# Kernel tuning notes

Hardware: AMD Instinct MI355X
Metric: run time of the kernel (lower is better)

The kernel has to match this reference:

```python
import jax, jax.numpy as jnp
import numpy as np

N_NODES = 50000
N_EDGES = 800000
D = 128          # input_dim == output_dim
H = 2 * D        # hidden size = 2*output_dim
EPS = 1e-5       # BatchNorm1d eps


def _mlp(x, W1, b1, g1, beta1, W2, b2):
    # Linear -> BatchNorm1d (training-mode batch stats) -> ReLU -> Linear
    y = x @ W1 + b1
    mu = jnp.mean(y, axis=0)
    var = jnp.mean(jnp.square(y - mu), axis=0)  # biased var, as used for normalization
    y = (y - mu) * jax.lax.rsqrt(var + EPS) * g1 + beta1
    y = jax.nn.relu(y)
    return y @ W2 + b2


def setup_inputs() -> dict:
    key = jax.random.key(0)
    ks = jax.random.split(key, 16)
    h = jax.random.normal(ks[0], (N_NODES, D), dtype=jnp.float32)
    e = jax.random.normal(ks[1], (N_EDGES, D), dtype=jnp.float32)
    src = jax.random.randint(ks[2], (N_EDGES,), 0, N_NODES, dtype=jnp.int32)
    dst = jax.random.randint(ks[3], (N_EDGES,), 0, N_NODES, dtype=jnp.int32)

    def lin(k, fan_in, fan_out):
        return jax.random.normal(k, (fan_in, fan_out), dtype=jnp.float32) * (1.0 / np.sqrt(fan_in))

    params = {
        # mlp_bond: in 2D -> H -> D
        'W1b': lin(ks[4], 2 * D, H), 'b1b': jnp.zeros((H,), jnp.float32),
        'g1b': jnp.ones((H,), jnp.float32), 'beta1b': jnp.zeros((H,), jnp.float32),
        'W2b': lin(ks[5], H, D), 'b2b': jnp.zeros((D,), jnp.float32),
        # mlp_atom: in 2D -> H -> D
        'W1a': lin(ks[6], 2 * D, H), 'b1a': jnp.zeros((H,), jnp.float32),
        'g1a': jnp.ones((H,), jnp.float32), 'beta1a': jnp.zeros((H,), jnp.float32),
        'W2a': lin(ks[7], H, D), 'b2a': jnp.zeros((D,), jnp.float32),
    }
    return {'h': h, 'e': e, 'src': src, 'dst': dst, **params}


def reference(h, e, src, dst,
              W1b, b1b, g1b, beta1b, W2b, b2b,
              W1a, b1a, g1a, beta1a, W2a, b2a):
    # --- bond update: gather u_add_v, concat with e, MLP ---
    sum_h_edge = h[src] + h[dst]                              # [E, D]
    e_new = _mlp(jnp.concatenate([sum_h_edge, e], axis=-1),
                 W1b, b1b, g1b, beta1b, W2b, b2b)             # [E, D]

    # --- atom update: scatter-sum of src node feats and NEW edge feats to dst ---
    sum_h = jax.ops.segment_sum(h[src], dst, num_segments=N_NODES)   # copy_u + sum
    sum_e = jax.ops.segment_sum(e_new, dst, num_segments=N_NODES)   # copy_e + sum
    h_new = _mlp(jnp.concatenate([sum_h, sum_e], axis=-1),
                 W1a, b1a, g1a, beta1a, W2a, b2a)             # [N, D]

    # out_batch_norm=False, out_activation=None, residual=False, dropout=None
    return h_new, e_new
```

## Files before the change

### kernel.cpp

```cpp
#include <hip/hip_runtime.h>
#include <stdint.h>

#define DD 128
#define HH 256
#define EPSBN 1e-5f

typedef __attribute__((ext_vector_type(4))) float f32x4;
typedef __attribute__((ext_vector_type(8))) short s16x8;
typedef __attribute__((ext_vector_type(4))) short s16x4;

__device__ __forceinline__ unsigned short f2bf(float f){
  union{float f; unsigned u;} v; v.f=f;
  unsigned u = v.u + 0x7fffu + ((v.u>>16)&1u);
  return (unsigned short)(u>>16);
}
__device__ __forceinline__ float bf2f(unsigned short s){
  union{unsigned u; float f;} v; v.u=((unsigned)s)<<16; return v.f;
}
__device__ __forceinline__ int swz(int row, int kb){ return row*512 + (kb ^ ((row&7)<<4)); }

__global__ void wt_kernel(const float* __restrict__ W1b, const float* __restrict__ W2b,
                          const float* __restrict__ W1a, const float* __restrict__ W2a,
                          unsigned short* __restrict__ WT1b, unsigned short* __restrict__ WT2b,
                          unsigned short* __restrict__ WT1a, unsigned short* __restrict__ WT2a){
  int idx = blockIdx.x*256 + threadIdx.x;
  if (idx < 65536){ int n=idx>>8, k=idx&255; WT1b[n*256+k]=f2bf(W1b[k*256+n]); }
  else if (idx < 98304){ int t=idx-65536; int n=t>>8, k=t&255; WT2b[n*256+k]=f2bf(W2b[k*128+n]); }
  else if (idx < 163840){ int t=idx-98304; int n=t>>8, k=t&255; WT1a[n*256+k]=f2bf(W1a[k*256+n]); }
  else if (idx < 196608){ int t=idx-163840; int n=t>>8, k=t&255; WT2a[n*256+k]=f2bf(W2a[k*128+n]); }
}

__global__ void h2bf_kernel(const float* __restrict__ h, unsigned short* __restrict__ hb, int n8){
  int i = blockIdx.x*256 + threadIdx.x;
  if (i < n8){
    f32x4 a = *(const f32x4*)(h + (size_t)i*8);
    f32x4 b = *(const f32x4*)(h + (size_t)i*8 + 4);
    s16x8 p;
    #pragma unroll
    for (int q=0;q<4;q++){ p[q]=(short)f2bf(a[q]); p[4+q]=(short)f2bf(b[q]); }
    *(s16x8*)(hb + (size_t)i*8) = p;
  }
}

__global__ void hist_kernel(const int* __restrict__ dst, int* __restrict__ counts, int E){
  int i = blockIdx.x*256 + threadIdx.x;
  if (i < E) atomicAdd(&counts[dst[i]], 1);
}

__global__ void scan_kernel(const int* __restrict__ counts, int* __restrict__ offsets,
                            int* __restrict__ cursor, int n){
  __shared__ int wsum[16];
  int tid = threadIdx.x, lane = tid&63, wid = tid>>6;
  int carry = 0;
  int nch = (n + 1023)/1024;
  for (int ch=0; ch<nch; ch++){
    int i = ch*1024 + tid;
    int v = (i<n)? counts[i] : 0;
    int s = v;
    #pragma unroll
    for (int off=1; off<64; off<<=1){ int t = __shfl_up(s, off); if (lane>=off) s += t; }
    if (lane==63) wsum[wid] = s;
    __syncthreads();
    int woff = 0, tot = 0;
    #pragma unroll
    for (int w=0; w<16; w++){ int t = wsum[w]; if (w<wid) woff += t; tot += t; }
    if (i<n){ int excl = carry + woff + s - v; offsets[i]=excl; cursor[i]=excl; }
    carry += tot;
    __syncthreads();
  }
  if (tid==0) offsets[n] = carry;
}

__global__ void fill_kernel(const int* __restrict__ dst, int* __restrict__ cursor,
                            int* __restrict__ eids, int E){
  int i = blockIdx.x*256 + threadIdx.x;
  if (i < E){ int slot = atomicAdd(&cursor[dst[i]], 1); eids[slot] = i; }
}

__global__ __launch_bounds__(512, 4) void edge_mlp1_stream(
    const unsigned short* __restrict__ hb, const float* __restrict__ e,
    const int* __restrict__ src, const int* __restrict__ dstv,
    const unsigned short* __restrict__ WT1, const float* __restrict__ b1,
    unsigned short* __restrict__ yout, float* __restrict__ stats,
    int E, int ntiles)
{
  __shared__ alignas(16) char xt[32768];
  const int tid = threadIdx.x;
  const int l = tid&63, w = tid>>6, lr = l&15, lg = l>>4;
  const int nb = w*32;

  s16x8 Bf[8][2];
  #pragma unroll
  for (int kc=0;kc<8;kc++)
    #pragma unroll
    for (int nt=0;nt<2;nt++)
      Bf[kc][nt] = *(const s16x8*)(WT1 + (size_t)(nb + nt*16 + lr)*256 + kc*32 + lg*8);
  float bias0 = b1[nb+lr], bias1 = b1[nb+16+lr];

  float st1a=0.f, st1b=0.f, st2a=0.f, st2b=0.f;

  for (int t = blockIdx.x; t < ntiles; t += gridDim.x){
    const int base = t*64;
    {
      const int cb = tid&31, r0 = tid>>5;
      #pragma unroll
      for (int k=0;k<4;k++){
        int r = r0 + k*16;
        f32x4 v = *(const f32x4*)(e + (size_t)(base+r)*DD + cb*4);
        s16x4 p;
        #pragma unroll
        for (int q=0;q<4;q++) p[q] = (short)f2bf(v[q]);
        *(s16x4*)(xt + swz(r, 256 + cb*8)) = p;
      }
    }
    {
      const int r = tid>>3, jj = tid&7;
      const int ei = base + r;
      int s_ = src[ei], d_ = dstv[ei];
      const s16x8* hs = (const s16x8*)(hb + (size_t)s_*DD) + jj*2;
      const s16x8* hd = (const s16x8*)(hb + (size_t)d_*DD) + jj*2;
      s16x8 a0=hs[0], a1=hs[1], c0=hd[0], c1=hd[1];
      s16x8 o0, o1;
      #pragma unroll
      for (int q=0;q<8;q++){
        o0[q] = (short)f2bf(bf2f((unsigned short)a0[q]) + bf2f((unsigned short)c0[q]));
        o1[q] = (short)f2bf(bf2f((unsigned short)a1[q]) + bf2f((unsigned short)c1[q]));
      }
      *(s16x8*)(xt + swz(r, jj*32))      = o0;
      *(s16x8*)(xt + swz(r, jj*32 + 16)) = o1;
    }
    __syncthreads();
    f32x4 acc[4][2];
    #pragma unroll
    for (int mt=0;mt<4;mt++)
      #pragma unroll
      for (int nt=0;nt<2;nt++) acc[mt][nt] = (f32x4){0.f,0.f,0.f,0.f};
    #pragma unroll
    for (int kc=0;kc<8;kc++){
      s16x8 af[4];
      #pragma unroll
      for (int mt=0;mt<4;mt++)
        af[mt] = *(const s16x8*)(xt + swz(mt*16 + lr, kc*64 + lg*16));
      #pragma unroll
      for (int nt=0;nt<2;nt++)
        #pragma unroll
        for (int mt=0;mt<4;mt++)
          acc[mt][nt] = __builtin_amdgcn_mfma_f32_16x16x32_bf16(af[mt], Bf[kc][nt], acc[mt][nt], 0,0,0);
    }
    #pragma unroll
    for (int mt=0;mt<4;mt++)
      #pragma unroll
      for (int q=0;q<4;q++){
        float v0 = acc[mt][0][q] + bias0;
        float v1 = acc[mt][1][q] + bias1;
        st1a += v0; st2a += v0*v0;
        st1b += v1; st2b += v1*v1;
      }
    __syncthreads();
    #pragma unroll
    for (int mt=0;mt<4;mt++)
      #pragma unroll
      for (int q=0;q<4;q++){
        *(unsigned short*)(xt + (mt*16 + lg*4 + q)*512 + (nb + lr)*2)      = f2bf(acc[mt][0][q] + bias0);
        *(unsigned short*)(xt + (mt*16 + lg*4 + q)*512 + (nb + 16 + lr)*2) = f2bf(acc[mt][1][q] + bias1);
      }
    __syncthreads();
    #pragma unroll
    for (int it=0;it<4;it++){
      int off = it*8192 + tid*16;
      *(s16x8*)((char*)yout + (size_t)base*512 + off) = *(const s16x8*)(xt + off);
    }
    __syncthreads();
  }
  {
    int rep = blockIdx.x & 63;
    float s;
    s = st1a; s += __shfl_xor(s,16); s += __shfl_xor(s,32);
    if (l < 16) atomicAdd(&stats[rep*512 + nb + lr], s);
    s = st2a; s += __shfl_xor(s,16); s += __shfl_xor(s,32);
    if (l < 16) atomicAdd(&stats[rep*512 + 256 + nb + lr], s);
    s = st1b; s += __shfl_xor(s,16); s += __shfl_xor(s,32);
    if (l < 16) atomicAdd(&stats[rep*512 + nb + 16 + lr], s);
    s = st2b; s += __shfl_xor(s,16); s += __shfl_xor(s,32);
    if (l < 16) atomicAdd(&stats[rep*512 + 256 + nb + 16 + lr], s);
  }
}

__device__ __forceinline__ void gemm256_epilogue(char* xt, const unsigned short* __restrict__ WT,
                                                 const float* __restrict__ b1,
                                                 unsigned short* __restrict__ yout,
                                                 float* __restrict__ stats,
                                                 int base, int nrows_total)
{
  const int tid = threadIdx.x;
  const int l = tid&63, w = tid>>6, lr = l&15, lg = l>>4;
  const int nbase = w*64;
  f32x4 acc[4][4];
  #pragma unroll
  for (int nt=0; nt<4; nt++){
    float bv = b1[nbase + nt*16 + lr];
    #pragma unroll
    for (int mt=0; mt<4; mt++) acc[mt][nt] = (f32x4){bv,bv,bv,bv};
  }
  #pragma unroll
  for (int kc=0; kc<8; kc++){
    s16x8 af[4];
    #pragma unroll
    for (int mt=0; mt<4; mt++){
      int row = mt*16 + lr;
      af[mt] = *(const s16x8*)(xt + swz(row, kc*64 + lg*16));
    }
    s16x8 bfr[4];
    #pragma unroll
    for (int nt=0; nt<4; nt++)
      bfr[nt] = *(const s16x8*)(WT + (size_t)(nbase + nt*16 + lr)*256 + kc*32 + lg*8);
    #pragma unroll
    for (int nt=0; nt<4; nt++)
      #pragma unroll
      for (int mt=0; mt<4; mt++)
        acc[mt][nt] = __builtin_amdgcn_mfma_f32_16x16x32_bf16(af[mt], bfr[nt], acc[mt][nt], 0,0,0);
  }
  {
    int rep = blockIdx.x & 63;
    #pragma unroll
    for (int nt=0; nt<4; nt++){
      float s1=0.f, s2=0.f;
      #pragma unroll
      for (int mt=0; mt<4; mt++){
        #pragma unroll
        for (int q=0; q<4; q++){
          float v = acc[mt][nt][q];
          float m = (base + mt*16 + lg*4 + q < nrows_total) ? 1.0f : 0.0f;
          v *= m;
          s1 += v; s2 += v*v;
        }
      }
      s1 += __shfl_xor(s1,16); s1 += __shfl_xor(s1,32);
      s2 += __shfl_xor(s2,16); s2 += __shfl_xor(s2,32);
      if (l < 16){
        int col = nbase + nt*16 + lr;
        atomicAdd(&stats[rep*512 + col],       s1);
        atomicAdd(&stats[rep*512 + 256 + col], s2);
      }
    }
  }
  __syncthreads();
  #pragma unroll
  for (int mt=0; mt<4; mt++)
    #pragma unroll
    for (int nt=0; nt<4; nt++)
      #pragma unroll
      for (int q=0; q<4; q++)
        *(unsigned short*)(xt + (mt*16 + lg*4 + q)*512 + (nbase + nt*16 + lr)*2) = f2bf(acc[mt][nt][q]);
  __syncthreads();
  #pragma unroll
  for (int it=0; it<8; it++){
    int off = it*4096 + tid*16;
    int row = off >> 9;
    if (base + row < nrows_total)
      *(s16x8*)((char*)yout + (size_t)base*512 + off) = *(const s16x8*)(xt + off);
  }
}

__global__ __launch_bounds__(256) void node_mlp1(const unsigned short* __restrict__ hb, const float* __restrict__ enew,
    const int* __restrict__ src, const int* __restrict__ offsets, const int* __restrict__ eids,
    const unsigned short* __restrict__ WT1, const float* __restrict__ b1,
    unsigned short* __restrict__ yout, float* __restrict__ stats, int NN)
{
  __shared__ alignas(16) char xt[32768];
  const int tid = threadIdx.x;
  const int base = blockIdx.x*64;
  const int r = tid>>2, j = tid&3;
  const int node = base + r;
  float ah[4][8];
  f32x4 ae[8];
  #pragma unroll
  for (int c=0;c<4;c++)
    #pragma unroll
    for (int q=0;q<8;q++) ah[c][q]=0.f;
  #pragma unroll
  for (int c=0;c<8;c++) ae[c]=(f32x4){0,0,0,0};
  if (node < NN){
    int beg = offsets[node], end = offsets[node+1];
    for (int p=beg;p<end;p++){
      int eid = eids[p];
      int s = src[eid];
      const s16x8* hs = (const s16x8*)(hb + (size_t)s*DD);
      const f32x4* ep = (const f32x4*)(enew + (size_t)eid*DD);
      #pragma unroll
      for (int c=0;c<4;c++){
        s16x8 a = hs[c*4+j];
        #pragma unroll
        for (int q=0;q<8;q++) ah[c][q] += bf2f((unsigned short)a[q]);
      }
      #pragma unroll
      for (int c=0;c<8;c++) ae[c] += ep[c*4+j];
    }
  }
  #pragma unroll
  for (int c=0;c<4;c++){
    s16x8 o;
    #pragma unroll
    for (int q=0;q<8;q++) o[q] = (short)f2bf(ah[c][q]);
    *(s16x8*)(xt + swz(r, (c*4+j)*16)) = o;
  }
  #pragma unroll
  for (int c=0;c<8;c++){
    s16x4 p;
    #pragma unroll
    for (int q=0;q<4;q++) p[q] = (short)f2bf(ae[c][q]);
    *(s16x4*)(xt + swz(r, 256 + (c*4+j)*8)) = p;
  }
  __syncthreads();
  gemm256_epilogue(xt, WT1, b1, yout, stats, base, NN);
}

__global__ void finalize_kernel(const float* __restrict__ stats, const float* __restrict__ g,
                                const float* __restrict__ beta, float* __restrict__ scale, float invcnt){
  __shared__ float red[512];
  int tid = threadIdx.x;
  float s = 0.f;
  for (int rep=0; rep<64; rep++) s += stats[rep*512 + tid];
  red[tid] = s;
  __syncthreads();
  if (tid < 256){
    float mu  = red[tid]*invcnt;
    float var = red[256+tid]*invcnt - mu*mu;
    float a = g[tid] * rsqrtf(var + EPSBN);
    float c = beta[tid] - mu*a;
    scale[2*tid] = a; scale[2*tid+1] = c;
  }
}

__global__ __launch_bounds__(512, 4) void mlp2_stream(const unsigned short* y,
    const unsigned short* __restrict__ WT2, const float* __restrict__ b2,
    const float* __restrict__ scale, float* outp, int nrows, int ntiles)
{
  __shared__ alignas(16) char xt[32768];
  const int tid = threadIdx.x;
  const int l = tid&63, w = tid>>6, lr = l&15, lg = l>>4;
  const int nb = w*16;

  s16x8 Bf[8];
  #pragma unroll
  for (int kc=0;kc<8;kc++)
    Bf[kc] = *(const s16x8*)(WT2 + (size_t)(nb + lr)*HH + kc*32 + lg*8);
  float bias = b2[nb+lr];

  const int cb = tid&31, r0 = tid>>5;
  float sa[8], sc[8];
  #pragma unroll
  for (int q=0;q<8;q++){ sa[q]=scale[2*(cb*8+q)]; sc[q]=scale[2*(cb*8+q)+1]; }

  for (int t = blockIdx.x; t < ntiles; t += gridDim.x){
    const int base = t*64;
    #pragma unroll
    for (int k=0;k<4;k++){
      int r = r0 + k*16;
      s16x8 raw = {0,0,0,0,0,0,0,0};
      if (base + r < nrows) raw = *(const s16x8*)(y + (size_t)(base+r)*HH + cb*8);
      s16x8 o;
      #pragma unroll
      for (int q=0;q<8;q++){
        float f = fmaxf(bf2f((unsigned short)raw[q])*sa[q] + sc[q], 0.0f);
        o[q] = (short)f2bf(f);
      }
      *(s16x8*)(xt + swz(r, cb*16)) = o;
    }
    __syncthreads();
    f32x4 acc[4];
    #pragma unroll
    for (int mt=0;mt<4;mt++) acc[mt] = (f32x4){0.f,0.f,0.f,0.f};
    #pragma unroll
    for (int kc=0;kc<8;kc++){
      s16x8 af[4];
      #pragma unroll
      for (int mt=0;mt<4;mt++)
        af[mt] = *(const s16x8*)(xt + swz(mt*16 + lr, kc*64 + lg*16));
      #pragma unroll
      for (int mt=0;mt<4;mt++)
        acc[mt] = __builtin_amdgcn_mfma_f32_16x16x32_bf16(af[mt], Bf[kc], acc[mt], 0,0,0);
    }
    __syncthreads();
    #pragma unroll
    for (int mt=0;mt<4;mt++)
      #pragma unroll
      for (int q=0;q<4;q++)
        *(float*)(xt + (mt*16 + lg*4 + q)*512 + (nb + lr)*4) = acc[mt][q] + bias;
    __syncthreads();
    #pragma unroll
    for (int it=0;it<4;it++){
      int off = it*8192 + tid*16;
      int row = off >> 9;
      if (base + row < nrows)
        *(f32x4*)(outp + (size_t)(base+row)*DD + ((off&511)>>2)) = *(const f32x4*)(xt + off);
    }
    __syncthreads();
  }
}

extern "C" void kernel_launch(void* const* d_in, const int* in_sizes, int n_in,
                              void* d_out, int out_size, void* d_ws, size_t ws_size,
                              hipStream_t stream) {
  const float* h    = (const float*)d_in[0];
  const float* e    = (const float*)d_in[1];
  const int*   src  = (const int*)d_in[2];
  const int*   dst  = (const int*)d_in[3];
  const float* W1b  = (const float*)d_in[4];
  const float* b1b  = (const float*)d_in[5];
  const float* g1b  = (const float*)d_in[6];
  const float* beta1b=(const float*)d_in[7];
  const float* W2b  = (const float*)d_in[8];
  const float* b2b  = (const float*)d_in[9];
  const float* W1a  = (const float*)d_in[10];
  const float* b1a  = (const float*)d_in[11];
  const float* g1a  = (const float*)d_in[12];
  const float* beta1a=(const float*)d_in[13];
  const float* W2a  = (const float*)d_in[14];
  const float* b2a  = (const float*)d_in[15];

  const int E  = in_sizes[2];
  const int NN = in_sizes[0] / DD;

  char* ws = (char*)d_ws;
  unsigned short* WT1b = (unsigned short*)(ws + 0);
  unsigned short* WT2b = (unsigned short*)(ws + 131072);
  unsigned short* WT1a = (unsigned short*)(ws + 196608);
  unsigned short* WT2a = (unsigned short*)(ws + 327680);
  float* scaleE = (float*)(ws + 393216);
  float* scaleN = (float*)(ws + 395264);
  float* statsE = (float*)(ws + 397312);
  float* statsN = (float*)(ws + 528384);
  int* counts  = (int*)(ws + 659456);
  int* offsets = (int*)(ws + 860160);
  int* cursor  = (int*)(ws + 1060864);
  int* eids    = (int*)(ws + 1261568);
  unsigned short* ya = (unsigned short*)(ws + 4461568);
  unsigned short* hb = (unsigned short*)(ws + 30086144);

  float* outH = (float*)d_out;
  float* outE = outH + (size_t)NN * DD;
  unsigned short* yE = (unsigned short*)outE;

  hipMemsetAsync(ws + 397312, 0, 131072 + 131072 + 200704, stream);

  wt_kernel<<<768, 256, 0, stream>>>(W1b, W2b, W1a, W2a, WT1b, WT2b, WT1a, WT2a);
  h2bf_kernel<<<(NN*DD/8 + 255)/256, 256, 0, stream>>>(h, hb, NN*DD/8);
  hist_kernel<<<(E+255)/256, 256, 0, stream>>>(dst, counts, E);
  scan_kernel<<<1, 1024, 0, stream>>>(counts, offsets, cursor, NN);
  fill_kernel<<<(E+255)/256, 256, 0, stream>>>(dst, cursor, eids, E);

  const int tE = E/64;
  const int tN = (NN + 63)/64;
  const int gridE = (tE < 2048) ? tE : 2048;

  edge_mlp1_stream<<<gridE, 512, 0, stream>>>(hb, e, src, dst, WT1b, b1b, yE, statsE, E, tE);
  finalize_kernel<<<1, 512, 0, stream>>>(statsE, g1b, beta1b, scaleE, 1.0f/(float)E);
  mlp2_stream<<<gridE, 512, 0, stream>>>(yE, WT2b, b2b, scaleE, outE, E, tE);
  node_mlp1<<<tN, 256, 0, stream>>>(hb, outE, src, offsets, eids, WT1a, b1a, ya, statsN, NN);
  finalize_kernel<<<1, 512, 0, stream>>>(statsN, g1a, beta1a, scaleN, 1.0f/(float)NN);
  mlp2_stream<<<tN, 512, 0, stream>>>(ya, WT2a, b2a, scaleN, outH, NN, tN);
}
```

Before: 887.6 us.

## Replace persistent grid-stride loops with one-tile-per-block kernels and widen node gather

The edge MLP1 and MLP2 kernels stop running as persistent grid-stride loops and launch one 64-row tile per block. Each block now loads its weight fragments after issuing the input gathers, so the weight loads can overlap the gathers. The node aggregation kernel moves to 512 threads, with 8 threads per node each covering 16 contiguous columns, and it shares a common register-resident GEMM core with the edge kernel. The trade-off is that every block reloads weights and issues its own stats atomics (12500 blocks instead of 2048), in exchange for more parallelism and better latency hiding.

```diff
diff --git a/kernel.cpp b/kernel.cpp
--- a/kernel.cpp
+++ b/kernel.cpp
@@ -77,100 +77,58 @@
   if (i < E){ int slot = atomicAdd(&cursor[dst[i]], 1); eids[slot] = i; }
 }
 
-__global__ __launch_bounds__(512, 4) void edge_mlp1_stream(
-    const unsigned short* __restrict__ hb, const float* __restrict__ e,
-    const int* __restrict__ src, const int* __restrict__ dstv,
-    const unsigned short* __restrict__ WT1, const float* __restrict__ b1,
-    unsigned short* __restrict__ yout, float* __restrict__ stats,
-    int E, int ntiles)
+__device__ __forceinline__ void gemm1_core(char* xt, const s16x8 (&Bf)[8][2],
+                                           float bias0, float bias1,
+                                           unsigned short* __restrict__ yout,
+                                           float* __restrict__ stats,
+                                           int base, int nrows)
 {
-  __shared__ alignas(16) char xt[32768];
   const int tid = threadIdx.x;
   const int l = tid&63, w = tid>>6, lr = l&15, lg = l>>4;
   const int nb = w*32;
-
-  s16x8 Bf[8][2];
-  #pragma unroll
-  for (int kc=0;kc<8;kc++)
+  f32x4 acc[4][2];
+  #pragma unroll
+  for (int mt=0;mt<4;mt++)
+    #pragma unroll
+    for (int nt=0;nt<2;nt++) acc[mt][nt] = (f32x4){0.f,0.f,0.f,0.f};
+  #pragma unroll
+  for (int kc=0;kc<8;kc++){
+    s16x8 af[4];
+    #pragma unroll
+    for (int mt=0;mt<4;mt++)
+      af[mt] = *(const s16x8*)(xt + swz(mt*16 + lr, kc*64 + lg*16));
     #pragma unroll
     for (int nt=0;nt<2;nt++)
-      Bf[kc][nt] = *(const s16x8*)(WT1 + (size_t)(nb + nt*16 + lr)*256 + kc*32 + lg*8);
-  float bias0 = b1[nb+lr], bias1 = b1[nb+16+lr];
-
-  float st1a=0.f, st1b=0.f, st2a=0.f, st2b=0.f;
-
-  for (int t = blockIdx.x; t < ntiles; t += gridDim.x){
-    const int base = t*64;
-    {
-      const int cb = tid&31, r0 = tid>>5;
-      #pragma unroll
-      for (int k=0;k<4;k++){
-        int r = r0 + k*16;
-        f32x4 v = *(const f32x4*)(e + (size_t)(base+r)*DD + cb*4);
-        s16x4 p;
-        #pragma unroll
-        for (int q=0;q<4;q++) p[q] = (short)f2bf(v[q]);
-        *(s16x4*)(xt + swz(r, 256 + cb*8)) = p;
-      }
-    }
-    {
-      const int r = tid>>3, jj = tid&7;
-      const int ei = base + r;
-      int s_ = src[ei], d_ = dstv[ei];
-      const s16x8* hs = (const s16x8*)(hb + (size_t)s_*DD) + jj*2;
-      const s16x8* hd = (const s16x8*)(hb + (size_t)d_*DD) + jj*2;
-      s16x8 a0=hs[0], a1=hs[1], c0=hd[0], c1=hd[1];
-      s16x8 o0, o1;
-      #pragma unroll
-      for (int q=0;q<8;q++){
-        o0[q] = (short)f2bf(bf2f((unsigned short)a0[q]) + bf2f((unsigned short)c0[q]));
-        o1[q] = (short)f2bf(bf2f((unsigned short)a1[q]) + bf2f((unsigned short)c1[q]));
-      }
-      *(s16x8*)(xt + swz(r, jj*32))      = o0;
-      *(s16x8*)(xt + swz(r, jj*32 + 16)) = o1;
-    }
-    __syncthreads();
-    f32x4 acc[4][2];
-    #pragma unroll
-    for (int mt=0;mt<4;mt++)
-      #pragma unroll
-      for (int nt=0;nt<2;nt++) acc[mt][nt] = (f32x4){0.f,0.f,0.f,0.f};
-    #pragma unroll
-    for (int kc=0;kc<8;kc++){
-      s16x8 af[4];
       #pragma unroll
       for (int mt=0;mt<4;mt++)
-        af[mt] = *(const s16x8*)(xt + swz(mt*16 + lr, kc*64 + lg*16));
-      #pragma unroll
-      for (int nt=0;nt<2;nt++)
-        #pragma unroll
-        for (int mt=0;mt<4;mt++)
-          acc[mt][nt] = __builtin_amdgcn_mfma_f32_16x16x32_bf16(af[mt], Bf[kc][nt], acc[mt][nt], 0,0,0);
-    }
-    #pragma unroll
-    for (int mt=0;mt<4;mt++)
-      #pragma unroll
-      for (int q=0;q<4;q++){
-        float v0 = acc[mt][0][q] + bias0;
-        float v1 = acc[mt][1][q] + bias1;
-        st1a += v0; st2a += v0*v0;
-        st1b += v1; st2b += v1*v1;
-      }
-    __syncthreads();
-    #pragma unroll
-    for (int mt=0;mt<4;mt++)
-      #pragma unroll
-      for (int q=0;q<4;q++){
-        *(unsigned short*)(xt + (mt*16 + lg*4 + q)*512 + (nb + lr)*2)      = f2bf(acc[mt][0][q] + bias0);
-        *(unsigned short*)(xt + (mt*16 + lg*4 + q)*512 + (nb + 16 + lr)*2) = f2bf(acc[mt][1][q] + bias1);
-      }
-    __syncthreads();
-    #pragma unroll
-    for (int it=0;it<4;it++){
-      int off = it*8192 + tid*16;
+        acc[mt][nt] = __builtin_amdgcn_mfma_f32_16x16x32_bf16(af[mt], Bf[kc][nt], acc[mt][nt], 0,0,0);
+  }
+  float st1a=0.f, st1b=0.f, st2a=0.f, st2b=0.f;
+  #pragma unroll
+  for (int mt=0;mt<4;mt++)
+    #pragma unroll
+    for (int q=0;q<4;q++){
+      float m = (base + mt*16 + lg*4 + q < nrows) ? 1.0f : 0.0f;
+      float v0 = (acc[mt][0][q] + bias0)*m;
+      float v1 = (acc[mt][1][q] + bias1)*m;
+      st1a += v0; st2a += v0*v0;
+      st1b += v1; st2b += v1*v1;
+    }
+  __syncthreads();
+  #pragma unroll
+  for (int mt=0;mt<4;mt++)
+    #pragma unroll
+    for (int q=0;q<4;q++){
+      *(unsigned short*)(xt + (mt*16 + lg*4 + q)*512 + (nb + lr)*2)      = f2bf(acc[mt][0][q] + bias0);
+      *(unsigned short*)(xt + (mt*16 + lg*4 + q)*512 + (nb + 16 + lr)*2) = f2bf(acc[mt][1][q] + bias1);
+    }
+  __syncthreads();
+  #pragma unroll
+  for (int it=0;it<4;it++){
+    int off = it*8192 + tid*16;
+    int row = off >> 9;
+    if (base + row < nrows)
       *(s16x8*)((char*)yout + (size_t)base*512 + off) = *(const s16x8*)(xt + off);
-    }
-    __syncthreads();
   }
   {
     int rep = blockIdx.x & 63;
@@ -186,133 +144,109 @@
   }
 }
 
-__device__ __forceinline__ void gemm256_epilogue(char* xt, const unsigned short* __restrict__ WT,
-                                                 const float* __restrict__ b1,
-                                                 unsigned short* __restrict__ yout,
-                                                 float* __restrict__ stats,
-                                                 int base, int nrows_total)
+__global__ __launch_bounds__(512, 4) void edge_mlp1(
+    const unsigned short* __restrict__ hb, const float* __restrict__ e,
+    const int* __restrict__ src, const int* __restrict__ dstv,
+    const unsigned short* __restrict__ WT1, const float* __restrict__ b1,
+    unsigned short* __restrict__ yout, float* __restrict__ stats, int E)
 {
+  __shared__ alignas(16) char xt[32768];
   const int tid = threadIdx.x;
   const int l = tid&63, w = tid>>6, lr = l&15, lg = l>>4;
-  const int nbase = w*64;
-  f32x4 acc[4][4];
-  #pragma unroll
-  for (int nt=0; nt<4; nt++){
-    float bv = b1[nbase + nt*16 + lr];
-    #pragma unroll
-    for (int mt=0; mt<4; mt++) acc[mt][nt] = (f32x4){bv,bv,bv,bv};
-  }
-  #pragma unroll
-  for (int kc=0; kc<8; kc++){
-    s16x8 af[4];
-    #pragma unroll
-    for (int mt=0; mt<4; mt++){
-      int row = mt*16 + lr;
-      af[mt] = *(const s16x8*)(xt + swz(row, kc*64 + lg*16));
-    }
-    s16x8 bfr[4];
-    #pragma unroll
-    for (int nt=0; nt<4; nt++)
-      bfr[nt] = *(const s16x8*)(WT + (size_t)(nbase + nt*16 + lr)*256 + kc*32 + lg*8);
-    #pragma unroll
-    for (int nt=0; nt<4; nt++)
+  const int nb = w*32;
+  const int base = blockIdx.x*64;
+
+  {
+    const int cb = tid&31, r0 = tid>>5;
+    #pragma unroll
+    for (int k=0;k<4;k++){
+      int r = r0 + k*16;
+      f32x4 v = *(const f32x4*)(e + (size_t)(base+r)*DD + cb*4);
+      s16x4 p;
       #pragma unroll
-      for (int mt=0; mt<4; mt++)
-        acc[mt][nt] = __builtin_amdgcn_mfma_f32_16x16x32_bf16(af[mt], bfr[nt], acc[mt][nt], 0,0,0);
+      for (int q=0;q<4;q++) p[q] = (short)f2bf(v[q]);
+      *(s16x4*)(xt + swz(r, 256 + cb*8)) = p;
+    }
   }
   {
-    int rep = blockIdx.x & 63;
-    #pragma unroll
-    for (int nt=0; nt<4; nt++){
-      float s1=0.f, s2=0.f;
-      #pragma unroll
-      for (int mt=0; mt<4; mt++){
-        #pragma unroll
-        for (int q=0; q<4; q++){
-          float v = acc[mt][nt][q];
-          float m = (base + mt*16 + lg*4 + q < nrows_total) ? 1.0f : 0.0f;
-          v *= m;
-          s1 += v; s2 += v*v;
-        }
-      }
-      s1 += __shfl_xor(s1,16); s1 += __shfl_xor(s1,32);
-      s2 += __shfl_xor(s2,16); s2 += __shfl_xor(s2,32);
-      if (l < 16){
-        int col = nbase + nt*16 + lr;
-        atomicAdd(&stats[rep*512 + col],       s1);
-        atomicAdd(&stats[rep*512 + 256 + col], s2);
-      }
-    }
-  }
-  __syncthreads();
-  #pragma unroll
-  for (int mt=0; mt<4; mt++)
-    #pragma unroll
-    for (int nt=0; nt<4; nt++)
-      #pragma unroll
-      for (int q=0; q<4; q++)
-        *(unsigned short*)(xt + (mt*16 + lg*4 + q)*512 + (nbase + nt*16 + lr)*2) = f2bf(acc[mt][nt][q]);
-  __syncthreads();
-  #pragma unroll
-  for (int it=0; it<8; it++){
-    int off = it*4096 + tid*16;
-    int row = off >> 9;
-    if (base + row < nrows_total)
-      *(s16x8*)((char*)yout + (size_t)base*512 + off) = *(const s16x8*)(xt + off);
-  }
-}
-
-__global__ __launch_bounds__(256) void node_mlp1(const unsigned short* __restrict__ hb, const float* __restrict__ enew,
+    const int r = tid>>3, jj = tid&7;
+    const int ei = base + r;
+    int s_ = src[ei], d_ = dstv[ei];
+    const s16x8* hs = (const s16x8*)(hb + (size_t)s_*DD) + jj*2;
+    const s16x8* hd = (const s16x8*)(hb + (size_t)d_*DD) + jj*2;
+    s16x8 a0=hs[0], a1=hs[1], c0=hd[0], c1=hd[1];
+    s16x8 o0, o1;
+    #pragma unroll
+    for (int q=0;q<8;q++){
+      o0[q] = (short)f2bf(bf2f((unsigned short)a0[q]) + bf2f((unsigned short)c0[q]));
+      o1[q] = (short)f2bf(bf2f((unsigned short)a1[q]) + bf2f((unsigned short)c1[q]));
+    }
+    *(s16x8*)(xt + swz(r, jj*32))      = o0;
+    *(s16x8*)(xt + swz(r, jj*32 + 16)) = o1;
+  }
+  s16x8 Bf[8][2];
+  #pragma unroll
+  for (int kc=0;kc<8;kc++)
+    #pragma unroll
+    for (int nt=0;nt<2;nt++)
+      Bf[kc][nt] = *(const s16x8*)(WT1 + (size_t)(nb + nt*16 + lr)*256 + kc*32 + lg*8);
+  float bias0 = b1[nb+lr], bias1 = b1[nb+16+lr];
+  __syncthreads();
+  gemm1_core(xt, Bf, bias0, bias1, yout, stats, base, E);
+}
+
+__global__ __launch_bounds__(512, 2) void node_mlp1(
+    const unsigned short* __restrict__ hb, const float* __restrict__ enew,
     const int* __restrict__ src, const int* __restrict__ offsets, const int* __restrict__ eids,
     const unsigned short* __restrict__ WT1, const float* __restrict__ b1,
     unsigned short* __restrict__ yout, float* __restrict__ stats, int NN)
 {
   __shared__ alignas(16) char xt[32768];
   const int tid = threadIdx.x;
+  const int l = tid&63, w = tid>>6, lr = l&15, lg = l>>4;
+  const int nb = w*32;
   const int base = blockIdx.x*64;
-  const int r = tid>>2, j = tid&3;
+  const int r = tid>>3, jj = tid&7;
   const int node = base + r;
-  float ah[4][8];
-  f32x4 ae[8];
-  #pragma unroll
-  for (int c=0;c<4;c++)
-    #pragma unroll
-    for (int q=0;q<8;q++) ah[c][q]=0.f;
-  #pragma unroll
-  for (int c=0;c<8;c++) ae[c]=(f32x4){0,0,0,0};
+
+  float ah[16], ae[16];
+  #pragma unroll
+  for (int q=0;q<16;q++){ ah[q]=0.f; ae[q]=0.f; }
   if (node < NN){
     int beg = offsets[node], end = offsets[node+1];
     for (int p=beg;p<end;p++){
       int eid = eids[p];
-      int s = src[eid];
-      const s16x8* hs = (const s16x8*)(hb + (size_t)s*DD);
-      const f32x4* ep = (const f32x4*)(enew + (size_t)eid*DD);
+      int s_ = src[eid];
+      const s16x8* hs = (const s16x8*)(hb + (size_t)s_*DD + jj*16);
+      const f32x4* ep = (const f32x4*)(enew + (size_t)eid*DD + jj*16);
+      s16x8 a0 = hs[0], a1 = hs[1];
+      f32x4 e0 = ep[0], e1 = ep[1], e2 = ep[2], e3 = ep[3];
       #pragma unroll
-      for (int c=0;c<4;c++){
-        s16x8 a = hs[c*4+j];
-        #pragma unroll
-        for (int q=0;q<8;q++) ah[c][q] += bf2f((unsigned short)a[q]);
-      }
+      for (int q=0;q<8;q++){ ah[q] += bf2f((unsigned short)a0[q]); ah[8+q] += bf2f((unsigned short)a1[q]); }
       #pragma unroll
-      for (int c=0;c<8;c++) ae[c] += ep[c*4+j];
-    }
-  }
-  #pragma unroll
-  for (int c=0;c<4;c++){
-    s16x8 o;
-    #pragma unroll
-    for (int q=0;q<8;q++) o[q] = (short)f2bf(ah[c][q]);
-    *(s16x8*)(xt + swz(r, (c*4+j)*16)) = o;
-  }
-  #pragma unroll
-  for (int c=0;c<8;c++){
-    s16x4 p;
-    #pragma unroll
-    for (int q=0;q<4;q++) p[q] = (short)f2bf(ae[c][q]);
-    *(s16x4*)(xt + swz(r, 256 + (c*4+j)*8)) = p;
-  }
-  __syncthreads();
-  gemm256_epilogue(xt, WT1, b1, yout, stats, base, NN);
+      for (int q=0;q<4;q++){ ae[q] += e0[q]; ae[4+q] += e1[q]; ae[8+q] += e2[q]; ae[12+q] += e3[q]; }
+    }
+  }
+  {
+    s16x8 o0, o1;
+    #pragma unroll
+    for (int q=0;q<8;q++){ o0[q] = (short)f2bf(ah[q]); o1[q] = (short)f2bf(ah[8+q]); }
+    *(s16x8*)(xt + swz(r, jj*32))      = o0;
+    *(s16x8*)(xt + swz(r, jj*32 + 16)) = o1;
+    #pragma unroll
+    for (int q=0;q<8;q++){ o0[q] = (short)f2bf(ae[q]); o1[q] = (short)f2bf(ae[8+q]); }
+    *(s16x8*)(xt + swz(r, 256 + jj*32))      = o0;
+    *(s16x8*)(xt + swz(r, 256 + jj*32 + 16)) = o1;
+  }
+  s16x8 Bf[8][2];
+  #pragma unroll
+  for (int kc=0;kc<8;kc++)
+    #pragma unroll
+    for (int nt=0;nt<2;nt++)
+      Bf[kc][nt] = *(const s16x8*)(WT1 + (size_t)(nb + nt*16 + lr)*256 + kc*32 + lg*8);
+  float bias0 = b1[nb+lr], bias1 = b1[nb+16+lr];
+  __syncthreads();
+  gemm1_core(xt, Bf, bias0, bias1, yout, stats, base, NN);
 }
 
 __global__ void finalize_kernel(const float* __restrict__ stats, const float* __restrict__ g,
@@ -332,70 +266,66 @@
   }
 }
 
-__global__ __launch_bounds__(512, 4) void mlp2_stream(const unsigned short* y,
+__global__ __launch_bounds__(512, 4) void mlp2_kernel(const unsigned short* y,
     const unsigned short* __restrict__ WT2, const float* __restrict__ b2,
-    const float* __restrict__ scale, float* outp, int nrows, int ntiles)
+    const float* __restrict__ scale, float* outp, int nrows)
 {
   __shared__ alignas(16) char xt[32768];
   const int tid = threadIdx.x;
   const int l = tid&63, w = tid>>6, lr = l&15, lg = l>>4;
   const int nb = w*16;
-
+  const int base = blockIdx.x*64;
+
+  const int cb = tid&31, r0 = tid>>5;
+  float sa[8], sc[8];
+  #pragma unroll
+  for (int q=0;q<8;q++){ sa[q]=scale[2*(cb*8+q)]; sc[q]=scale[2*(cb*8+q)+1]; }
+  #pragma unroll
+  for (int k=0;k<4;k++){
+    int r = r0 + k*16;
+    s16x8 raw = {0,0,0,0,0,0,0,0};
+    if (base + r < nrows) raw = *(const s16x8*)(y + (size_t)(base+r)*HH + cb*8);
+    s16x8 o;
+    #pragma unroll
+    for (int q=0;q<8;q++){
+      float f = fmaxf(bf2f((unsigned short)raw[q])*sa[q] + sc[q], 0.0f);
+      o[q] = (short)f2bf(f);
+    }
+    *(s16x8*)(xt + swz(r, cb*16)) = o;
+  }
   s16x8 Bf[8];
   #pragma unroll
   for (int kc=0;kc<8;kc++)
     Bf[kc] = *(const s16x8*)(WT2 + (size_t)(nb + lr)*HH + kc*32 + lg*8);
   float bias = b2[nb+lr];
-
-  const int cb = tid&31, r0 = tid>>5;
-  float sa[8], sc[8];
-  #pragma unroll
-  for (int q=0;q<8;q++){ sa[q]=scale[2*(cb*8+q)]; sc[q]=scale[2*(cb*8+q)+1]; }
-
-  for (int t = blockIdx.x; t < ntiles; t += gridDim.x){
-    const int base = t*64;
-    #pragma unroll
-    for (int k=0;k<4;k++){
-      int r = r0 + k*16;
-      s16x8 raw = {0,0,0,0,0,0,0,0};
-      if (base + r < nrows) raw = *(const s16x8*)(y + (size_t)(base+r)*HH + cb*8);
-      s16x8 o;
-      #pragma unroll
-      for (int q=0;q<8;q++){
-        float f = fmaxf(bf2f((unsigned short)raw[q])*sa[q] + sc[q], 0.0f);
-        o[q] = (short)f2bf(f);
-      }
-      *(s16x8*)(xt + swz(r, cb*16)) = o;
-    }
-    __syncthreads();
-    f32x4 acc[4];
-    #pragma unroll
-    for (int mt=0;mt<4;mt++) acc[mt] = (f32x4){0.f,0.f,0.f,0.f};
-    #pragma unroll
-    for (int kc=0;kc<8;kc++){
-      s16x8 af[4];
-      #pragma unroll
-      for (int mt=0;mt<4;mt++)
-        af[mt] = *(const s16x8*)(xt + swz(mt*16 + lr, kc*64 + lg*16));
-      #pragma unroll
-      for (int mt=0;mt<4;mt++)
-        acc[mt] = __builtin_amdgcn_mfma_f32_16x16x32_bf16(af[mt], Bf[kc], acc[mt], 0,0,0);
-    }
-    __syncthreads();
+  __syncthreads();
+
+  f32x4 acc[4];
+  #pragma unroll
+  for (int mt=0;mt<4;mt++) acc[mt] = (f32x4){0.f,0.f,0.f,0.f};
+  #pragma unroll
+  for (int kc=0;kc<8;kc++){
+    s16x8 af[4];
     #pragma unroll
     for (int mt=0;mt<4;mt++)
-      #pragma unroll
-      for (int q=0;q<4;q++)
-        *(float*)(xt + (mt*16 + lg*4 + q)*512 + (nb + lr)*4) = acc[mt][q] + bias;
-    __syncthreads();
-    #pragma unroll
-    for (int it=0;it<4;it++){
-      int off = it*8192 + tid*16;
-      int row = off >> 9;
-      if (base + row < nrows)
-        *(f32x4*)(outp + (size_t)(base+row)*DD + ((off&511)>>2)) = *(const f32x4*)(xt + off);
-    }
-    __syncthreads();
+      af[mt] = *(const s16x8*)(xt + swz(mt*16 + lr, kc*64 + lg*16));
+    #pragma unroll
+    for (int mt=0;mt<4;mt++)
+      acc[mt] = __builtin_amdgcn_mfma_f32_16x16x32_bf16(af[mt], Bf[kc], acc[mt], 0,0,0);
+  }
+  __syncthreads();
+  #pragma unroll
+  for (int mt=0;mt<4;mt++)
+    #pragma unroll
+    for (int q=0;q<4;q++)
+      *(float*)(xt + (mt*16 + lg*4 + q)*512 + (nb + lr)*4) = acc[mt][q] + bias;
+  __syncthreads();
+  #pragma unroll
+  for (int it=0;it<4;it++){
+    int off = it*8192 + tid*16;
+    int row = off >> 9;
+    if (base + row < nrows)
+      *(f32x4*)(outp + (size_t)(base+row)*DD + ((off&511)>>2)) = *(const f32x4*)(xt + off);
   }
 }
 
@@ -452,12 +382,11 @@
 
   const int tE = E/64;
   const int tN = (NN + 63)/64;
-  const int gridE = (tE < 2048) ? tE : 2048;
-
-  edge_mlp1_stream<<<gridE, 512, 0, stream>>>(hb, e, src, dst, WT1b, b1b, yE, statsE, E, tE);
+
+  edge_mlp1<<<tE, 512, 0, stream>>>(hb, e, src, dst, WT1b, b1b, yE, statsE, E);
   finalize_kernel<<<1, 512, 0, stream>>>(statsE, g1b, beta1b, scaleE, 1.0f/(float)E);
-  mlp2_stream<<<gridE, 512, 0, stream>>>(yE, WT2b, b2b, scaleE, outE, E, tE);
-  node_mlp1<<<tN, 256, 0, stream>>>(hb, outE, src, offsets, eids, WT1a, b1a, ya, statsN, NN);
+  mlp2_kernel<<<tE, 512, 0, stream>>>(yE, WT2b, b2b, scaleE, outE, E);
+  node_mlp1<<<tN, 512, 0, stream>>>(hb, outE, src, offsets, eids, WT1a, b1a, ya, statsN, NN);
   finalize_kernel<<<1, 512, 0, stream>>>(statsN, g1a, beta1a, scaleN, 1.0f/(float)NN);
-  mlp2_stream<<<tN, 512, 0, stream>>>(ya, WT2a, b2a, scaleN, outH, NN, tN);
-}
+  mlp2_kernel<<<tN, 512, 0, stream>>>(ya, WT2a, b2a, scaleN, outH, NN);
+}
```

After: 800.5 us. 9.8% less time.
